# Kernel tuning notes

Measured on AMD Instinct MI355X. Metric: run time of the kernel, lower is better.

Reference implementation:

```python
import jax, jax.numpy as jnp
import numpy as np

N = 100000        # nodes
E = 1600000       # edges (avg degree 16)
D_IN = 128        # input_dim
HID = 128         # hidden
L = 2             # num_layers
EPS = 1e-5        # LayerNorm eps (torch default)


def setup_inputs() -> dict:
    key = jax.random.key(0)
    ks = jax.random.split(key, 5)
    x = jax.random.normal(ks[0], (N, D_IN), dtype=jnp.float32)
    edge_index = jax.random.randint(ks[1], (2, E), 0, N, dtype=jnp.int64)
    e_feat = jax.random.uniform(ks[2], (E,), dtype=jnp.float32)
    # nn.Linear(input_dim, hidden): weight [hidden, input_dim], bias [hidden]
    lin_w = jax.random.normal(ks[3], (HID, D_IN), dtype=jnp.float32) / np.float32(np.sqrt(D_IN))
    lin_b = jax.random.normal(ks[4], (HID,), dtype=jnp.float32) * 0.01
    ln_scale = jnp.ones((L, HID), dtype=jnp.float32)
    ln_bias = jnp.zeros((L, HID), dtype=jnp.float32)
    return {"x": x, "edge_index": edge_index, "e_feat": e_feat,
            "lin_w": lin_w, "lin_b": lin_b,
            "ln_scale": ln_scale, "ln_bias": ln_bias}


def _layernorm(h, scale, bias):
    mu = jnp.mean(h, axis=-1, keepdims=True)
    var = jnp.mean(jnp.square(h - mu), axis=-1, keepdims=True)
    return (h - mu) * jax.lax.rsqrt(var + EPS) * scale + bias


def reference(x, edge_index, e_feat, lin_w, lin_b, ln_scale, ln_bias):
    src, dst = edge_index[0], edge_index[1]
    h = x @ lin_w.T + lin_b            # [N, HID]
    ori = h
    for i in range(L):
        if i != 0:                      # res=True
            h = h + ori
        h = _layernorm(h, ln_scale[i], ln_bias[i])   # norm=True
        h = jax.nn.relu(h)              # relu=True; dp=0 -> dropout no-op
        # GraphConv(weight=False, bias=False): weighted SpMM aggregation
        msg = h[src] * e_feat[:, None]  # [E, HID]
        h = jax.ops.segment_sum(msg, dst, num_segments=N)  # [N, HID]
    return h
```

## Files before the change

kernel.cpp:

```cpp
#include <hip/hip_runtime.h>


constexpr int N_NODES = 100000;
constexpr int N_EDGES = 1600000;
constexpr int HID     = 128;
constexpr int NBKT    = (N_NODES + 511) / 512;
constexpr int BCAP    = 9216;
constexpr float LN_EPS = 1e-5f;

typedef __attribute__((ext_vector_type(8))) short short8;
typedef __attribute__((ext_vector_type(4))) float floatx4;

__device__ inline unsigned pack_bf16x2(float a, float b) {
    unsigned ua = __float_as_uint(a), ub = __float_as_uint(b);
    ua += 0x7fff + ((ua >> 16) & 1);
    ub += 0x7fff + ((ub >> 16) & 1);
    return (ua >> 16) | (ub & 0xffff0000u);
}
__device__ inline float bflo(unsigned u) { return __uint_as_float(u << 16); }
__device__ inline float bfhi(unsigned u) { return __uint_as_float(u & 0xffff0000u); }

__global__ __launch_bounds__(256) void k_bin(const int* __restrict__ ei,
                                             const float* __restrict__ ef,
                                             int* __restrict__ gcur,
                                             int* __restrict__ gbufDst,
                                             int2* __restrict__ gbufSW) {
    __shared__ int cnt[NBKT];
    __shared__ int incl[256];
    __shared__ int gbase[NBKT];
    __shared__ int sdst[2048];
    __shared__ int2 ssw[2048];
    const int t = threadIdx.x;

    for (int e0 = blockIdx.x * 2048; e0 < N_EDGES; e0 += gridDim.x * 2048) {
        for (int i = t; i < NBKT; i += 256) cnt[i] = 0;
        __syncthreads();

        const int nE = min(2048, N_EDGES - e0);
        int ed[8], es[8], ep[8]; float ew[8];
        const int base = e0 + t * 8;
        if (base + 8 <= N_EDGES) {
            int4 s0 = *(const int4*)&ei[base];
            int4 s1 = *(const int4*)&ei[base + 4];
            int4 d0 = *(const int4*)&ei[N_EDGES + base];
            int4 d1 = *(const int4*)&ei[N_EDGES + base + 4];
            float4 w0 = *(const float4*)&ef[base];
            float4 w1 = *(const float4*)&ef[base + 4];
            es[0]=s0.x; es[1]=s0.y; es[2]=s0.z; es[3]=s0.w;
            es[4]=s1.x; es[5]=s1.y; es[6]=s1.z; es[7]=s1.w;
            ed[0]=d0.x; ed[1]=d0.y; ed[2]=d0.z; ed[3]=d0.w;
            ed[4]=d1.x; ed[5]=d1.y; ed[6]=d1.z; ed[7]=d1.w;
            ew[0]=w0.x; ew[1]=w0.y; ew[2]=w0.z; ew[3]=w0.w;
            ew[4]=w1.x; ew[5]=w1.y; ew[6]=w1.z; ew[7]=w1.w;
#pragma unroll
            for (int k = 0; k < 8; ++k) ep[k] = atomicAdd(&cnt[ed[k] >> 9], 1);
        } else {
#pragma unroll
            for (int k = 0; k < 8; ++k) {
                int idx = base + k;
                if (idx < N_EDGES) {
                    es[k] = ei[idx]; ed[k] = ei[N_EDGES + idx]; ew[k] = ef[idx];
                    ep[k] = atomicAdd(&cnt[ed[k] >> 9], 1);
                } else ed[k] = -1;
            }
        }
        __syncthreads();

        int v = (t < NBKT) ? cnt[t] : 0;
        incl[t] = v;
        for (int o = 1; o < 256; o <<= 1) {
            __syncthreads();
            int u = (t >= o) ? incl[t - o] : 0;
            __syncthreads();
            incl[t] += u;
        }
        __syncthreads();
        if (t < NBKT) gbase[t] = atomicAdd(&gcur[t], v);
        __syncthreads();

#pragma unroll
        for (int k = 0; k < 8; ++k) {
            if (ed[k] < 0) continue;
            int b = ed[k] >> 9;
            int idx = incl[b] - cnt[b] + ep[k];
            sdst[idx] = ed[k];
            ssw[idx] = make_int2(es[k], __float_as_int(ew[k]));
        }
        __syncthreads();

        for (int j = t; j < nE; j += 256) {
            int d = sdst[j];
            int b = d >> 9;
            int pos = gbase[b] + (j - (incl[b] - cnt[b]));
            if (pos < BCAP) {
                gbufDst[(size_t)b * BCAP + pos] = d;
                gbufSW [(size_t)b * BCAP + pos] = ssw[j];
            }
        }
        __syncthreads();
    }
}

__global__ __launch_bounds__(512) void k_build(const int* __restrict__ gcur,
                                               const int* __restrict__ gbufDst,
                                               const int2* __restrict__ gbufSW,
                                               int* __restrict__ rp,
                                               int2* __restrict__ csr) {
    __shared__ int cnt[512];
    __shared__ int cur[512];
    __shared__ int2 sorted[BCAP];
    const int t     = threadIdx.x;
    const int b     = blockIdx.x;
    const int nbase = b * 512;

    int v0 = (t < NBKT) ? min(gcur[t], BCAP) : 0;
    cnt[t] = v0;
    for (int o = 1; o < 512; o <<= 1) {
        __syncthreads();
        int u = (t >= o) ? cnt[t - o] : 0;
        __syncthreads();
        cnt[t] += u;
    }
    __syncthreads();
    const int nb = min(gcur[b], BCAP);
    const int cb = cnt[b] - nb;
    if (b == NBKT - 1 && t == 0) rp[N_NODES] = cnt[NBKT - 1];
    __syncthreads();

    const int*  bd = gbufDst + (size_t)b * BCAP;
    const int2* bs = gbufSW  + (size_t)b * BCAP;

    cnt[t] = 0;
    __syncthreads();
    for (int i = t; i < nb; i += 512) atomicAdd(&cnt[bd[i] - nbase], 1);
    __syncthreads();

    int v = cnt[t];
    for (int o = 1; o < 512; o <<= 1) {
        __syncthreads();
        int u = (t >= o) ? cnt[t - o] : 0;
        __syncthreads();
        cnt[t] += u;
    }
    __syncthreads();
    const int excl = cnt[t] - v;
    cur[t] = excl;
    if (nbase + t < N_NODES) rp[nbase + t] = cb + excl;
    __syncthreads();

    for (int i = t; i < nb; i += 512) {
        int d = bd[i];
        int pos = atomicAdd(&cur[d - nbase], 1);
        sorted[pos] = bs[i];
    }
    __syncthreads();
    for (int i = t; i < nb; i += 512) csr[(size_t)cb + i] = sorted[i];
}

__global__ __launch_bounds__(256) void k_gemm_mfma(const float* __restrict__ x,
                                                   const float* __restrict__ W,
                                                   const float* __restrict__ bias,
                                                   const float* __restrict__ lns,
                                                   const float* __restrict__ lnb,
                                                   unsigned* __restrict__ orib,
                                                   unsigned* __restrict__ hact) {
    __shared__ __align__(16) char smem[128 * 136 * 2 + 64 * 136 * 2];
    ushort (*Ws)[136] = (ushort(*)[136])smem;
    ushort (*Xs)[136] = (ushort(*)[136])(smem + 128 * 136 * 2);
    float  (*Hs)[132] = (float(*)[132])smem;

    const int t    = threadIdx.x;
    const int row0 = blockIdx.x * 64;

    {
        const float4* Wf = (const float4*)W;
#pragma unroll
        for (int i = 0; i < 8; ++i) {
            int g = t + 256 * i;
            float4 p = Wf[g * 2], q = Wf[g * 2 + 1];
            uint4 vv = make_uint4(pack_bf16x2(p.x, p.y), pack_bf16x2(p.z, p.w),
                                  pack_bf16x2(q.x, q.y), pack_bf16x2(q.z, q.w));
            int r = g >> 4;
            int c = (g & 15) * 8;
            *(uint4*)&Ws[r][c] = vv;
        }
    }
    {
        const float4* xg = (const float4*)x;
        const int base = blockIdx.x * 2048;
#pragma unroll
        for (int i = 0; i < 8; ++i) {
            int f = t + 256 * i;
            int g = base + f;
            float4 vv = make_float4(0.f, 0.f, 0.f, 0.f);
            if (g < N_NODES * 32) vv = xg[g];
            int r = f >> 5;
            int c = (f & 31) * 4;
            uint2 p = make_uint2(pack_bf16x2(vv.x, vv.y), pack_bf16x2(vv.z, vv.w));
            *(uint2*)&Xs[r][c] = p;
        }
    }
    __syncthreads();

    const int wv   = t >> 6;
    const int l    = t & 63;
    const int mrow = l & 15;
    const int kq   = l >> 4;

    floatx4 acc[8];
#pragma unroll
    for (int i = 0; i < 8; ++i) acc[i] = (floatx4){0.f, 0.f, 0.f, 0.f};

#pragma unroll
    for (int ks = 0; ks < 4; ++ks) {
        short8 a = *(const short8*)&Xs[wv * 16 + mrow][ks * 32 + kq * 8];
#pragma unroll
        for (int tc = 0; tc < 8; ++tc) {
            short8 bb = *(const short8*)&Ws[tc * 16 + mrow][ks * 32 + kq * 8];
            acc[tc] = __builtin_amdgcn_mfma_f32_16x16x32_bf16(a, bb, acc[tc], 0, 0, 0);
        }
    }
    __syncthreads();

#pragma unroll
    for (int tc = 0; tc < 8; ++tc)
#pragma unroll
        for (int r = 0; r < 4; ++r)
            Hs[wv * 16 + kq * 4 + r][tc * 16 + mrow] = acc[tc][r];
    __syncthreads();

    const float2 b2  = ((const float2*)bias)[l];
    const float2 sc2 = ((const float2*)lns)[l];
    const float2 bb2 = ((const float2*)lnb)[l];
    for (int rr = 0; rr < 16; ++rr) {
        const int lrow = wv * 16 + rr;
        const int grow = row0 + lrow;
        if (grow >= N_NODES) break;
        float2 vv = *(const float2*)&Hs[lrow][l * 2];
        vv.x += b2.x; vv.y += b2.y;
        orib[(size_t)grow * 64 + l] = pack_bf16x2(vv.x, vv.y);
        float s  = vv.x + vv.y;
        float s2 = vv.x * vv.x + vv.y * vv.y;
#pragma unroll
        for (int m = 1; m < 64; m <<= 1) {
            s  += __shfl_xor(s, m);
            s2 += __shfl_xor(s2, m);
        }
        const float mu   = s * (1.0f / 128.0f);
        const float var  = s2 * (1.0f / 128.0f) - mu * mu;
        const float rstd = rsqrtf(var + LN_EPS);
        float y0 = fmaxf((vv.x - mu) * rstd * sc2.x + bb2.x, 0.0f);
        float y1 = fmaxf((vv.y - mu) * rstd * sc2.y + bb2.y, 0.0f);
        hact[(size_t)grow * 64 + l] = pack_bf16x2(y0, y1);
    }
}

#define SPMM_ACC(cc)                                                      \
    {                                                                     \
        unsigned v = Hb[(size_t)(cc).x * 64 + lane];                      \
        float w = __int_as_float((cc).y);                                 \
        accx += w * bflo(v);                                              \
        accy += w * bfhi(v);                                              \
    }

__device__ inline void spmm_row(const int2* __restrict__ csr,
                                const unsigned* __restrict__ Hb,
                                int beg, int end, int lane,
                                float& accx, float& accy) {
    int e = beg;
    for (; e + 8 <= end; e += 8) {
        int2 c0 = csr[e],     c1 = csr[e + 1], c2 = csr[e + 2], c3 = csr[e + 3];
        int2 c4 = csr[e + 4], c5 = csr[e + 5], c6 = csr[e + 6], c7 = csr[e + 7];
        SPMM_ACC(c0) SPMM_ACC(c1) SPMM_ACC(c2) SPMM_ACC(c3)
        SPMM_ACC(c4) SPMM_ACC(c5) SPMM_ACC(c6) SPMM_ACC(c7)
    }
    for (; e + 2 <= end; e += 2) {
        int2 c0 = csr[e], c1 = csr[e + 1];
        SPMM_ACC(c0) SPMM_ACC(c1)
    }
    if (e < end) {
        int2 c0 = csr[e];
        SPMM_ACC(c0)
    }
}

__global__ __launch_bounds__(256) void k_spmm_ln(const int* __restrict__ rp,
                                                 const int2* __restrict__ csr,
                                                 const unsigned* __restrict__ Hb,
                                                 const unsigned* __restrict__ orib,
                                                 const float* __restrict__ lns,
                                                 const float* __restrict__ lnb,
                                                 unsigned* __restrict__ hout) {
    const int wid  = (blockIdx.x * 256 + threadIdx.x) >> 6;
    const int lane = threadIdx.x & 63;

    const int beg = __builtin_amdgcn_readfirstlane(rp[wid]);
    const int end = __builtin_amdgcn_readfirstlane(rp[wid + 1]);

    float accx = 0.f, accy = 0.f;
    spmm_row(csr, Hb, beg, end, lane, accx, accy);

    unsigned o = orib[(size_t)wid * 64 + lane];
    float vx = accx + bflo(o), vy = accy + bfhi(o);
    float s  = vx + vy;
    float s2 = vx * vx + vy * vy;
#pragma unroll
    for (int m = 1; m < 64; m <<= 1) {
        s  += __shfl_xor(s, m);
        s2 += __shfl_xor(s2, m);
    }
    const float mu   = s * (1.0f / 128.0f);
    const float var  = s2 * (1.0f / 128.0f) - mu * mu;
    const float rstd = rsqrtf(var + LN_EPS);
    const float2 sc = ((const float2*)lns)[lane];
    const float2 bb = ((const float2*)lnb)[lane];
    float y0 = fmaxf((vx - mu) * rstd * sc.x + bb.x, 0.0f);
    float y1 = fmaxf((vy - mu) * rstd * sc.y + bb.y, 0.0f);
    hout[(size_t)wid * 64 + lane] = pack_bf16x2(y0, y1);
}

__global__ __launch_bounds__(256) void k_spmm_out(const int* __restrict__ rp,
                                                  const int2* __restrict__ csr,
                                                  const unsigned* __restrict__ Hb,
                                                  float* __restrict__ out) {
    const int wid  = (blockIdx.x * 256 + threadIdx.x) >> 6;
    const int lane = threadIdx.x & 63;

    const int beg = __builtin_amdgcn_readfirstlane(rp[wid]);
    const int end = __builtin_amdgcn_readfirstlane(rp[wid + 1]);

    float accx = 0.f, accy = 0.f;
    spmm_row(csr, Hb, beg, end, lane, accx, accy);

    ((float2*)out)[(size_t)wid * 64 + lane] = make_float2(accx, accy);
}

extern "C" void kernel_launch(void* const* d_in, const int* in_sizes, int n_in,
                              void* d_out, int out_size, void* d_ws, size_t ws_size,
                              hipStream_t stream) {
    const float* x   = (const float*)d_in[0];
    const int*   ei  = (const int*)d_in[1];
    const float* ef  = (const float*)d_in[2];
    const float* W   = (const float*)d_in[3];
    const float* b   = (const float*)d_in[4];
    const float* lns = (const float*)d_in[5];
    const float* lnb = (const float*)d_in[6];
    float* out = (float*)d_out;

    unsigned* orib = (unsigned*)d_out;

    unsigned* hact  = (unsigned*)d_ws;
    unsigned* hact2 = hact + (size_t)N_NODES * 64;
    int2* csr    = (int2*)(hact2 + (size_t)N_NODES * 64);
    int2* gbufSW = csr + N_EDGES;
    int* gcur    = (int*)(gbufSW + (size_t)NBKT * BCAP);
    int* rp      = gcur + NBKT;
    int* gbufDst = rp + (N_NODES + 1);

    const int wb = N_NODES * 64 / 256;

    hipMemsetAsync(gcur, 0, NBKT * sizeof(int), stream);
    k_bin<<<256, 256, 0, stream>>>(ei, ef, gcur, gbufDst, gbufSW);
    k_build<<<NBKT, 512, 0, stream>>>(gcur, gbufDst, gbufSW, rp, csr);

    k_gemm_mfma<<<(N_NODES + 63) / 64, 256, 0, stream>>>(x, W, b, lns, lnb, orib, hact);

    k_spmm_ln<<<wb, 256, 0, stream>>>(rp, csr, hact, orib, lns + HID, lnb + HID, hact2);
    k_spmm_out<<<wb, 256, 0, stream>>>(rp, csr, hact2, out);
}
```

Baseline: 313.2 us.

## Pack edge records, pad CSR rows, and slice feature layout for SpMM gathers

Each edge record becomes one 32-bit word: the source index in 17 bits and the weight quantized to 15 bits. CSR rows are padded to multiples of four at fixed per-bucket strides and described by a packed rowinfo word. Hidden features are stored in 8 column slices so each SpMM block gathers from a smaller region, and each thread handles 8 nodes with 128-bit record loads. The fused SpMM+LayerNorm is split into an fp16 aggregation kernel plus a separate LN kernel, and k_bin gets more blocks. This cuts edge-record traffic and improves gather locality, at the cost of an extra kernel launch, an fp16 intermediate round trip, and lossy weight quantization.

```diff
diff --git a/kernel.cpp b/kernel.cpp
--- a/kernel.cpp
+++ b/kernel.cpp
@@ -1,4 +1,5 @@
 #include <hip/hip_runtime.h>
+#include <hip/hip_fp16.h>
 
 
 constexpr int N_NODES = 100000;
@@ -6,10 +7,13 @@
 constexpr int HID     = 128;
 constexpr int NBKT    = (N_NODES + 511) / 512;
 constexpr int BCAP    = 9216;
+constexpr int BSTRIDE = 11264;
 constexpr float LN_EPS = 1e-5f;
 
 typedef __attribute__((ext_vector_type(8))) short short8;
 typedef __attribute__((ext_vector_type(4))) float floatx4;
+typedef __attribute__((ext_vector_type(4))) unsigned u32x4;
+typedef __attribute__((ext_vector_type(2))) float f32x2;
 
 __device__ inline unsigned pack_bf16x2(float a, float b) {
     unsigned ua = __float_as_uint(a), ub = __float_as_uint(b);
@@ -24,12 +28,12 @@
                                              const float* __restrict__ ef,
                                              int* __restrict__ gcur,
                                              int* __restrict__ gbufDst,
-                                             int2* __restrict__ gbufSW) {
+                                             unsigned* __restrict__ gbufRec) {
     __shared__ int cnt[NBKT];
     __shared__ int incl[256];
     __shared__ int gbase[NBKT];
     __shared__ int sdst[2048];
-    __shared__ int2 ssw[2048];
+    __shared__ unsigned ssw[2048];
     const int t = threadIdx.x;
 
     for (int e0 = blockIdx.x * 2048; e0 < N_EDGES; e0 += gridDim.x * 2048) {
@@ -37,7 +41,7 @@
         __syncthreads();
 
         const int nE = min(2048, N_EDGES - e0);
-        int ed[8], es[8], ep[8]; float ew[8];
+        int ed[8], ep[8]; unsigned er[8];
         const int base = e0 + t * 8;
         if (base + 8 <= N_EDGES) {
             int4 s0 = *(const int4*)&ei[base];
@@ -46,6 +50,7 @@
             int4 d1 = *(const int4*)&ei[N_EDGES + base + 4];
             float4 w0 = *(const float4*)&ef[base];
             float4 w1 = *(const float4*)&ef[base + 4];
+            int es[8]; float ew[8];
             es[0]=s0.x; es[1]=s0.y; es[2]=s0.z; es[3]=s0.w;
             es[4]=s1.x; es[5]=s1.y; es[6]=s1.z; es[7]=s1.w;
             ed[0]=d0.x; ed[1]=d0.y; ed[2]=d0.z; ed[3]=d0.w;
@@ -53,13 +58,21 @@
             ew[0]=w0.x; ew[1]=w0.y; ew[2]=w0.z; ew[3]=w0.w;
             ew[4]=w1.x; ew[5]=w1.y; ew[6]=w1.z; ew[7]=w1.w;
 #pragma unroll
-            for (int k = 0; k < 8; ++k) ep[k] = atomicAdd(&cnt[ed[k] >> 9], 1);
+            for (int k = 0; k < 8; ++k) {
+                unsigned q = __float2uint_rn(ew[k] * 32768.0f);
+                if (q > 32767u) q = 32767u;
+                er[k] = (q << 17) | (unsigned)es[k];
+                ep[k] = atomicAdd(&cnt[ed[k] >> 9], 1);
+            }
         } else {
 #pragma unroll
             for (int k = 0; k < 8; ++k) {
                 int idx = base + k;
                 if (idx < N_EDGES) {
-                    es[k] = ei[idx]; ed[k] = ei[N_EDGES + idx]; ew[k] = ef[idx];
+                    int s = ei[idx]; ed[k] = ei[N_EDGES + idx];
+                    unsigned q = __float2uint_rn(ef[idx] * 32768.0f);
+                    if (q > 32767u) q = 32767u;
+                    er[k] = (q << 17) | (unsigned)s;
                     ep[k] = atomicAdd(&cnt[ed[k] >> 9], 1);
                 } else ed[k] = -1;
             }
@@ -84,7 +97,7 @@
             int b = ed[k] >> 9;
             int idx = incl[b] - cnt[b] + ep[k];
             sdst[idx] = ed[k];
-            ssw[idx] = make_int2(es[k], __float_as_int(ew[k]));
+            ssw[idx]  = er[k];
         }
         __syncthreads();
 
@@ -94,7 +107,7 @@
             int pos = gbase[b] + (j - (incl[b] - cnt[b]));
             if (pos < BCAP) {
                 gbufDst[(size_t)b * BCAP + pos] = d;
-                gbufSW [(size_t)b * BCAP + pos] = ssw[j];
+                gbufRec[(size_t)b * BCAP + pos] = ssw[j];
             }
         }
         __syncthreads();
@@ -103,49 +116,44 @@
 
 __global__ __launch_bounds__(512) void k_build(const int* __restrict__ gcur,
                                                const int* __restrict__ gbufDst,
-                                               const int2* __restrict__ gbufSW,
-                                               int* __restrict__ rp,
-                                               int2* __restrict__ csr) {
+                                               const unsigned* __restrict__ gbufRec,
+                                               unsigned* __restrict__ rowinfo,
+                                               unsigned* __restrict__ rec) {
     __shared__ int cnt[512];
     __shared__ int cur[512];
-    __shared__ int2 sorted[BCAP];
+    __shared__ unsigned sorted[BSTRIDE];
     const int t     = threadIdx.x;
     const int b     = blockIdx.x;
     const int nbase = b * 512;
-
-    int v0 = (t < NBKT) ? min(gcur[t], BCAP) : 0;
-    cnt[t] = v0;
+    const int nb    = min(gcur[b], BCAP);
+    const unsigned cb = (unsigned)b * (unsigned)BSTRIDE;
+
+    cnt[t] = 0;
+    for (int i = t; i < BSTRIDE; i += 512) sorted[i] = 0;
+    __syncthreads();
+
+    const int*      bd = gbufDst + (size_t)b * BCAP;
+    const unsigned* bs = gbufRec + (size_t)b * BCAP;
+
+    for (int i = t; i < nb; i += 512) atomicAdd(&cnt[bd[i] - nbase], 1);
+    __syncthreads();
+
+    const int deg = cnt[t];
+    int v = (deg + 3) & ~3;
+    cur[t] = v;
     for (int o = 1; o < 512; o <<= 1) {
         __syncthreads();
-        int u = (t >= o) ? cnt[t - o] : 0;
-        __syncthreads();
-        cnt[t] += u;
-    }
-    __syncthreads();
-    const int nb = min(gcur[b], BCAP);
-    const int cb = cnt[b] - nb;
-    if (b == NBKT - 1 && t == 0) rp[N_NODES] = cnt[NBKT - 1];
-    __syncthreads();
-
-    const int*  bd = gbufDst + (size_t)b * BCAP;
-    const int2* bs = gbufSW  + (size_t)b * BCAP;
-
-    cnt[t] = 0;
-    __syncthreads();
-    for (int i = t; i < nb; i += 512) atomicAdd(&cnt[bd[i] - nbase], 1);
-    __syncthreads();
-
-    int v = cnt[t];
-    for (int o = 1; o < 512; o <<= 1) {
-        __syncthreads();
-        int u = (t >= o) ? cnt[t - o] : 0;
-        __syncthreads();
-        cnt[t] += u;
-    }
-    __syncthreads();
-    const int excl = cnt[t] - v;
+        int u = (t >= o) ? cur[t - o] : 0;
+        __syncthreads();
+        cur[t] += u;
+    }
+    __syncthreads();
+    const int padTotal = cur[511];
+    const int excl = cur[t] - v;
+    __syncthreads();
     cur[t] = excl;
-    if (nbase + t < N_NODES) rp[nbase + t] = cb + excl;
+    if (nbase + t < N_NODES)
+        rowinfo[nbase + t] = ((cb + (unsigned)excl) << 10) | (unsigned)deg;
     __syncthreads();
 
     for (int i = t; i < nb; i += 512) {
@@ -154,7 +162,7 @@
         sorted[pos] = bs[i];
     }
     __syncthreads();
-    for (int i = t; i < nb; i += 512) csr[(size_t)cb + i] = sorted[i];
+    for (int i = t; i < padTotal; i += 512) rec[(size_t)cb + i] = sorted[i];
 }
 
 __global__ __launch_bounds__(256) void k_gemm_mfma(const float* __restrict__ x,
@@ -251,57 +259,83 @@
         const float rstd = rsqrtf(var + LN_EPS);
         float y0 = fmaxf((vv.x - mu) * rstd * sc2.x + bb2.x, 0.0f);
         float y1 = fmaxf((vv.y - mu) * rstd * sc2.y + bb2.y, 0.0f);
-        hact[(size_t)grow * 64 + l] = pack_bf16x2(y0, y1);
-    }
-}
-
-#define SPMM_ACC(cc)                                                      \
-    {                                                                     \
-        unsigned v = Hb[(size_t)(cc).x * 64 + lane];                      \
-        float w = __int_as_float((cc).y);                                 \
-        accx += w * bflo(v);                                              \
-        accy += w * bfhi(v);                                              \
-    }
-
-__device__ inline void spmm_row(const int2* __restrict__ csr,
-                                const unsigned* __restrict__ Hb,
-                                int beg, int end, int lane,
-                                float& accx, float& accy) {
-    int e = beg;
-    for (; e + 8 <= end; e += 8) {
-        int2 c0 = csr[e],     c1 = csr[e + 1], c2 = csr[e + 2], c3 = csr[e + 3];
-        int2 c4 = csr[e + 4], c5 = csr[e + 5], c6 = csr[e + 6], c7 = csr[e + 7];
-        SPMM_ACC(c0) SPMM_ACC(c1) SPMM_ACC(c2) SPMM_ACC(c3)
-        SPMM_ACC(c4) SPMM_ACC(c5) SPMM_ACC(c6) SPMM_ACC(c7)
-    }
-    for (; e + 2 <= end; e += 2) {
-        int2 c0 = csr[e], c1 = csr[e + 1];
-        SPMM_ACC(c0) SPMM_ACC(c1)
-    }
-    if (e < end) {
-        int2 c0 = csr[e];
-        SPMM_ACC(c0)
-    }
-}
-
-__global__ __launch_bounds__(256) void k_spmm_ln(const int* __restrict__ rp,
-                                                 const int2* __restrict__ csr,
-                                                 const unsigned* __restrict__ Hb,
-                                                 const unsigned* __restrict__ orib,
-                                                 const float* __restrict__ lns,
-                                                 const float* __restrict__ lnb,
-                                                 unsigned* __restrict__ hout) {
+        hact[(size_t)(l >> 3) * (size_t)(N_NODES * 8) + (size_t)grow * 8 + (l & 7)] =
+            pack_bf16x2(y0, y1);
+    }
+}
+
+__device__ inline void spmm_slice(const unsigned* __restrict__ rowinfo,
+                                  const unsigned* __restrict__ rec,
+                                  const unsigned* __restrict__ Hb,
+                                  float& ax, float& ay,
+                                  int& node, int& slice, int& col) {
+    const int lane = threadIdx.x & 63;
+    slice = blockIdx.x & 7;
+    const int nb = blockIdx.x >> 3;
+    const int wv = threadIdx.x >> 6;
+    const int sub = lane >> 3;
+    col = lane & 7;
+    node = nb * 32 + wv * 8 + sub;
+
+    const unsigned info = rowinfo[node];
+    const int myBeg = (int)(info >> 10);
+    const int myDeg = (int)(info & 1023u);
+    const unsigned* Hs = Hb + (size_t)slice * (size_t)(N_NODES * 8) + col;
+    const u32x4* recv = (const u32x4*)(rec + myBeg);
+
+    ax = 0.f; ay = 0.f;
+    for (int off = 0; __any(off < myDeg); off += 4) {
+        u32x4 R = {0u, 0u, 0u, 0u};
+        if (off < myDeg) R = __builtin_nontemporal_load(recv + (off >> 2));
+        unsigned v0 = Hs[(size_t)(R[0] & 0x1FFFFu) * 8u];
+        unsigned v1 = Hs[(size_t)(R[1] & 0x1FFFFu) * 8u];
+        unsigned v2 = Hs[(size_t)(R[2] & 0x1FFFFu) * 8u];
+        unsigned v3 = Hs[(size_t)(R[3] & 0x1FFFFu) * 8u];
+        float w0 = (float)(R[0] >> 17);
+        float w1 = (float)(R[1] >> 17);
+        float w2 = (float)(R[2] >> 17);
+        float w3 = (float)(R[3] >> 17);
+        ax = fmaf(w0, bflo(v0), ax); ay = fmaf(w0, bfhi(v0), ay);
+        ax = fmaf(w1, bflo(v1), ax); ay = fmaf(w1, bfhi(v1), ay);
+        ax = fmaf(w2, bflo(v2), ax); ay = fmaf(w2, bfhi(v2), ay);
+        ax = fmaf(w3, bflo(v3), ax); ay = fmaf(w3, bfhi(v3), ay);
+    }
+    ax *= 3.0517578125e-05f;
+    ay *= 3.0517578125e-05f;
+}
+
+__global__ __launch_bounds__(256) void k_spmm_agg(const unsigned* __restrict__ rowinfo,
+                                                  const unsigned* __restrict__ rec,
+                                                  const unsigned* __restrict__ Hb,
+                                                  unsigned* __restrict__ agg) {
+    float ax, ay; int node, slice, col;
+    spmm_slice(rowinfo, rec, Hb, ax, ay, node, slice, col);
+    unsigned u = (unsigned)__half_as_ushort(__float2half(ax)) |
+                 ((unsigned)__half_as_ushort(__float2half(ay)) << 16);
+    __builtin_nontemporal_store(u, agg + (size_t)node * 64 + slice * 8 + col);
+}
+
+__global__ __launch_bounds__(256) void k_spmm_f32(const unsigned* __restrict__ rowinfo,
+                                                  const unsigned* __restrict__ rec,
+                                                  const unsigned* __restrict__ Hb,
+                                                  float* __restrict__ out) {
+    float ax, ay; int node, slice, col;
+    spmm_slice(rowinfo, rec, Hb, ax, ay, node, slice, col);
+    f32x2 o2 = {ax, ay};
+    __builtin_nontemporal_store(o2, (f32x2*)out + (size_t)node * 64 + slice * 8 + col);
+}
+
+__global__ __launch_bounds__(256) void k_ln(const unsigned* __restrict__ agg,
+                                            const unsigned* __restrict__ orib,
+                                            const float* __restrict__ lns,
+                                            const float* __restrict__ lnb,
+                                            unsigned* __restrict__ hact2) {
     const int wid  = (blockIdx.x * 256 + threadIdx.x) >> 6;
     const int lane = threadIdx.x & 63;
-
-    const int beg = __builtin_amdgcn_readfirstlane(rp[wid]);
-    const int end = __builtin_amdgcn_readfirstlane(rp[wid + 1]);
-
-    float accx = 0.f, accy = 0.f;
-    spmm_row(csr, Hb, beg, end, lane, accx, accy);
-
+    unsigned a = agg[(size_t)wid * 64 + lane];
     unsigned o = orib[(size_t)wid * 64 + lane];
-    float vx = accx + bflo(o), vy = accy + bfhi(o);
+    float vx = __half2float(__ushort_as_half((unsigned short)(a & 0xffffu))) + bflo(o);
+    float vy = __half2float(__ushort_as_half((unsigned short)(a >> 16)))     + bfhi(o);
     float s  = vx + vy;
     float s2 = vx * vx + vy * vy;
 #pragma unroll
@@ -316,23 +350,8 @@
     const float2 bb = ((const float2*)lnb)[lane];
     float y0 = fmaxf((vx - mu) * rstd * sc.x + bb.x, 0.0f);
     float y1 = fmaxf((vy - mu) * rstd * sc.y + bb.y, 0.0f);
-    hout[(size_t)wid * 64 + lane] = pack_bf16x2(y0, y1);
-}
-
-__global__ __launch_bounds__(256) void k_spmm_out(const int* __restrict__ rp,
-                                                  const int2* __restrict__ csr,
-                                                  const unsigned* __restrict__ Hb,
-                                                  float* __restrict__ out) {
-    const int wid  = (blockIdx.x * 256 + threadIdx.x) >> 6;
-    const int lane = threadIdx.x & 63;
-
-    const int beg = __builtin_amdgcn_readfirstlane(rp[wid]);
-    const int end = __builtin_amdgcn_readfirstlane(rp[wid + 1]);
-
-    float accx = 0.f, accy = 0.f;
-    spmm_row(csr, Hb, beg, end, lane, accx, accy);
-
-    ((float2*)out)[(size_t)wid * 64 + lane] = make_float2(accx, accy);
+    hact2[(size_t)(lane >> 3) * (size_t)(N_NODES * 8) + (size_t)wid * 8 + (lane & 7)] =
+        pack_bf16x2(y0, y1);
 }
 
 extern "C" void kernel_launch(void* const* d_in, const int* in_sizes, int n_in,
@@ -348,23 +367,23 @@
     float* out = (float*)d_out;
 
     unsigned* orib = (unsigned*)d_out;
-
-    unsigned* hact  = (unsigned*)d_ws;
-    unsigned* hact2 = hact + (size_t)N_NODES * 64;
-    int2* csr    = (int2*)(hact2 + (size_t)N_NODES * 64);
-    int2* gbufSW = csr + N_EDGES;
-    int* gcur    = (int*)(gbufSW + (size_t)NBKT * BCAP);
-    int* rp      = gcur + NBKT;
-    int* gbufDst = rp + (N_NODES + 1);
-
-    const int wb = N_NODES * 64 / 256;
+    unsigned* agg  = (unsigned*)d_out + (size_t)N_NODES * 64;
+
+    unsigned* rec     = (unsigned*)d_ws;
+    unsigned* hact    = rec + (size_t)NBKT * BSTRIDE;
+    unsigned* hact2   = hact + (size_t)N_NODES * 64;
+    unsigned* gbufRec = hact2 + (size_t)N_NODES * 64;
+    int*      gcur    = (int*)(gbufRec + (size_t)NBKT * BCAP);
+    unsigned* rowinfo = (unsigned*)(gcur + NBKT);
+    int*      gbufDst = (int*)(rowinfo + N_NODES);
 
     hipMemsetAsync(gcur, 0, NBKT * sizeof(int), stream);
-    k_bin<<<256, 256, 0, stream>>>(ei, ef, gcur, gbufDst, gbufSW);
-    k_build<<<NBKT, 512, 0, stream>>>(gcur, gbufDst, gbufSW, rp, csr);
+    k_bin<<<782, 256, 0, stream>>>(ei, ef, gcur, gbufDst, gbufRec);
+    k_build<<<NBKT, 512, 0, stream>>>(gcur, gbufDst, gbufRec, rowinfo, rec);
 
     k_gemm_mfma<<<(N_NODES + 63) / 64, 256, 0, stream>>>(x, W, b, lns, lnb, orib, hact);
 
-    k_spmm_ln<<<wb, 256, 0, stream>>>(rp, csr, hact, orib, lns + HID, lnb + HID, hact2);
-    k_spmm_out<<<wb, 256, 0, stream>>>(rp, csr, hact2, out);
-}
+    k_spmm_agg<<<25000, 256, 0, stream>>>(rowinfo, rec, hact, agg);
+    k_ln<<<25000, 256, 0, stream>>>(agg, orib, lns + HID, lnb + HID, hact2);
+    k_spmm_f32<<<25000, 256, 0, stream>>>(rowinfo, rec, hact2, out);
+}
```

After: 507.1 us. 61.9% more time.
